# Optimization experiments

Measured on AMD Instinct MI355X. Metric: run time of the kernel, lower is better.

## Reference

```python
import jax, jax.numpy as jnp
import numpy as np

N, L, D, H = 2, 2048, 1024, 16
Dh = D // H          # 64
HIST = 2048          # history_len
SCALE = D ** 0.5     # note: module scales by sqrt(model_dim), not sqrt(head_dim)


def setup_inputs() -> dict:
    key = jax.random.key(0)
    ks = jax.random.split(key, 10)
    f = lambda k, s, sc=1.0: jax.random.normal(k, s, dtype=jnp.float32) * sc
    i = jnp.arange(L)
    causal = i[None, :] > i[:, None]            # mask future
    old = i[None, :] <= i[:, None] - HIST       # mask beyond history window
    mask = causal | old                          # True = masked, (L, L)
    return {
        "values": f(ks[0], (N, L, D)),
        "keys": f(ks[1], (N, L, D)),
        "query": f(ks[2], (N, L, D)),
        "origin_values": f(ks[3], (N, L, D)),
        "origin_keys": f(ks[4], (N, L, D)),
        "Wv": f(ks[5], (Dh, Dh), 0.1),
        "Wk": f(ks[6], (Dh, Dh), 0.1),
        "Wq": f(ks[7], (Dh, Dh), 0.1),
        "fc_w": f(ks[8], (D, D), 0.03),
        "fc_b": jnp.zeros((D,), dtype=jnp.float32),
        "mask": mask,
    }


def reference(values, keys, query, origin_values, origin_keys, Wv, Wk, Wq, fc_w, fc_b, mask):
    # forward(..., ref_sample=True): mfpca_attention path.
    # origin_keys/values are projected exactly as the prior ref_sample=False call stored them.
    split = lambda x: x.reshape(N, L, H, Dh)
    v = split(values) @ Wv.T        # (N, L, H, Dh)  torch Linear: x @ W^T, no bias
    k = split(keys) @ Wk.T
    q = split(query) @ Wq.T
    ov = split(origin_values) @ Wv.T
    ok = split(origin_keys) @ Wk.T

    energy = jnp.einsum('nqhd,nkhd->nhqk', q, ok)       # (N, H, L, L)
    samp_energy = jnp.einsum('nlhd,nlhd->nhl', q, k)    # (N, H, L)
    eye = jnp.eye(L, dtype=bool)
    # energy.diagonal().copy_(samp_energy)
    energy = jnp.where(eye, samp_energy[:, :, None, :], energy)
    energy = jnp.where(mask, jnp.float32(-1e20), energy)
    scores = jax.nn.softmax(energy / SCALE, axis=-1)
    diag_scores = jnp.diagonal(scores, axis1=2, axis2=3)    # (N, H, L)
    scores_nodiag = jnp.where(eye, 0.0, scores)
    # NOTE: original einsum output is indexed by l (not q) -- reproduced faithfully.
    origin_attention = jnp.einsum('nhql,nlhd->nlhd', scores_nodiag, ov)
    samp_attention = jnp.einsum('nhl,nlhd->nlhd', diag_scores, v)
    attention = (samp_attention + origin_attention).reshape(N, L, D)
    return attention @ fc_w.T + fc_b
```

## Files before the change

kernel.cpp:

```cpp
#include <hip/hip_runtime.h>

#define NB 2
#define LL 2048
#define DD 1024
#define HH 16
#define NHH (NB*HH)
#define LT (LL/64)
#define KT16 (LL/16)
#define CEXP 0.0450842200277801f

typedef __bf16 bf16x8 __attribute__((ext_vector_type(8)));
typedef unsigned short u16x8 __attribute__((ext_vector_type(8)));
typedef float f32x4 __attribute__((ext_vector_type(4)));

#define MFMA16 __builtin_amdgcn_mfma_f32_16x16x32_bf16
#define EXP2 __builtin_amdgcn_exp2f

__device__ __forceinline__ unsigned short f2bf(float f) {
    unsigned u = __float_as_uint(f);
    return (unsigned short)((u + 0x7fffu + ((u >> 16) & 1u)) >> 16);
}
__device__ __forceinline__ float bf2f(unsigned short u) {
    return __uint_as_float(((unsigned)u) << 16);
}
__device__ __forceinline__ bf16x8 ldfrag(const unsigned short* p) {
    return *reinterpret_cast<const bf16x8*>(p);
}
__device__ __forceinline__ bf16x8 cvt8v(float4 a, float4 b) {
    u16x8 u;
    u[0]=f2bf(a.x); u[1]=f2bf(a.y); u[2]=f2bf(a.z); u[3]=f2bf(a.w);
    u[4]=f2bf(b.x); u[5]=f2bf(b.y); u[6]=f2bf(b.z); u[7]=f2bf(b.w);
    return __builtin_bit_cast(bf16x8, u);
}
__device__ __forceinline__ ushort4 pack4(f32x4 d, float sc) {
    ushort4 o;
    o.x = f2bf(d[0]*sc); o.y = f2bf(d[1]*sc); o.z = f2bf(d[2]*sc); o.w = f2bf(d[3]*sc);
    return o;
}
__device__ __forceinline__ void gload16(const unsigned short* g, unsigned short* l) {
    __builtin_amdgcn_global_load_lds(
        (const __attribute__((address_space(1))) unsigned int*)g,
        (__attribute__((address_space(3))) unsigned int*)l, 16, 0, 0);
}

__global__ __launch_bounds__(256) void wcvt_kernel(
    const float* __restrict__ Wk, const float* __restrict__ Wq,
    const float* __restrict__ Wv, unsigned short* __restrict__ wfrag)
{
    const int s = blockIdx.x * 256 + threadIdx.x;
    const int m = s >> 9;
    const int rem = s & 511;
    const int f = rem >> 6;
    const int lane = rem & 63;
    const int n16 = lane & 15, quad = lane >> 4;
    const int mt = f >> 1, half = f & 1;
    const float* W = (m == 0) ? Wk : (m == 1) ? Wq : Wv;
    const float* p = W + (mt*16 + n16)*64 + quad*8 + half*32;
    float4 a = *reinterpret_cast<const float4*>(p);
    float4 b = *reinterpret_cast<const float4*>(p + 4);
    *reinterpret_cast<bf16x8*>(wfrag + (size_t)s * 8) = cvt8v(a, b);
}

__global__ __launch_bounds__(256) void proj_kernel(
    const float* __restrict__ values, const float* __restrict__ keys,
    const float* __restrict__ query,  const float* __restrict__ ovals,
    const float* __restrict__ okeys,  const unsigned short* __restrict__ wfrag,
    unsigned short* __restrict__ qb, unsigned short* __restrict__ okb,
    unsigned short* __restrict__ vb, unsigned short* __restrict__ ovb,
    float* __restrict__ ediag)
{
    const int t = threadIdx.x;
    const int w = t >> 6;
    const int lane = t & 63;
    const int n16 = lane & 15;
    const int quad = lane >> 4;
    const int h = blockIdx.y;
    const int row = blockIdx.x * 64 + w * 16 + n16;
    const int nn = row >> 11;
    const int ll = row & 2047;
    const size_t xoff  = (size_t)row * DD + h * 64 + quad * 8;
    const size_t qbase = (((size_t)(nn * HH + h)) * LL + ll) * 64;
    const size_t vbase = (size_t)row * DD + h * 64;

    if (blockIdx.z == 0) {
        const float4* kp = reinterpret_cast<const float4*>(keys  + xoff);
        const float4* qp = reinterpret_cast<const float4*>(query + xoff);
        const float4* op = reinterpret_cast<const float4*>(okeys + xoff);
        float4 k0 = kp[0], k1 = kp[1], k2 = kp[8], k3 = kp[9];
        float4 q0 = qp[0], q1 = qp[1], q2 = qp[8], q3 = qp[9];
        float4 o0 = op[0], o1 = op[1], o2 = op[8], o3 = op[9];
        bf16x8 wk[8], wq[8];
#pragma unroll
        for (int f = 0; f < 8; ++f) {
            wk[f] = ldfrag(wfrag + (size_t)(f * 64 + lane) * 8);
            wq[f] = ldfrag(wfrag + (size_t)((8 + f) * 64 + lane) * 8);
        }
        bf16x8 xk0 = cvt8v(k0, k1), xk1 = cvt8v(k2, k3);
        bf16x8 xq0 = cvt8v(q0, q1), xq1 = cvt8v(q2, q3);
        bf16x8 xo0 = cvt8v(o0, o1), xo1 = cvt8v(o2, o3);
        f32x4 ka[4], qa[4];
#pragma unroll
        for (int mt = 0; mt < 4; ++mt) {
            f32x4 d = {0.f,0.f,0.f,0.f};
            d = MFMA16(wk[mt*2], xk0, d, 0,0,0);
            ka[mt] = MFMA16(wk[mt*2+1], xk1, d, 0,0,0);
        }
#pragma unroll
        for (int mt = 0; mt < 4; ++mt) {
            f32x4 d = {0.f,0.f,0.f,0.f};
            d = MFMA16(wq[mt*2], xq0, d, 0,0,0);
            qa[mt] = MFMA16(wq[mt*2+1], xq1, d, 0,0,0);
            *reinterpret_cast<ushort4*>(qb + qbase + mt*16 + quad*4) = pack4(qa[mt], CEXP);
        }
#pragma unroll
        for (int mt = 0; mt < 4; ++mt) {
            f32x4 d = {0.f,0.f,0.f,0.f};
            d = MFMA16(wk[mt*2], xo0, d, 0,0,0);
            d = MFMA16(wk[mt*2+1], xo1, d, 0,0,0);
            *reinterpret_cast<ushort4*>(okb + qbase + mt*16 + quad*4) = pack4(d, 1.0f);
        }
        float p = 0.f;
#pragma unroll
        for (int mt = 0; mt < 4; ++mt)
            p += qa[mt][0]*ka[mt][0] + qa[mt][1]*ka[mt][1]
               + qa[mt][2]*ka[mt][2] + qa[mt][3]*ka[mt][3];
        p += __shfl_xor(p, 16);
        p += __shfl_xor(p, 32);
        if (lane < 16)
            ediag[((size_t)(nn * HH + h)) * LL + ll] = p;
    } else {
        const float4* vp = reinterpret_cast<const float4*>(values + xoff);
        const float4* op = reinterpret_cast<const float4*>(ovals  + xoff);
        float4 v0 = vp[0], v1 = vp[1], v2 = vp[8], v3 = vp[9];
        float4 o0 = op[0], o1 = op[1], o2 = op[8], o3 = op[9];
        bf16x8 wv[8];
#pragma unroll
        for (int f = 0; f < 8; ++f)
            wv[f] = ldfrag(wfrag + (size_t)((16 + f) * 64 + lane) * 8);
        bf16x8 xv0 = cvt8v(v0, v1), xv1 = cvt8v(v2, v3);
        bf16x8 xo0 = cvt8v(o0, o1), xo1 = cvt8v(o2, o3);
#pragma unroll
        for (int mt = 0; mt < 4; ++mt) {
            f32x4 d = {0.f,0.f,0.f,0.f};
            d = MFMA16(wv[mt*2], xv0, d, 0,0,0);
            d = MFMA16(wv[mt*2+1], xv1, d, 0,0,0);
            *reinterpret_cast<ushort4*>(vb + vbase + mt*16 + quad*4) = pack4(d, 1.0f);
        }
#pragma unroll
        for (int mt = 0; mt < 4; ++mt) {
            f32x4 d = {0.f,0.f,0.f,0.f};
            d = MFMA16(wv[mt*2], xo0, d, 0,0,0);
            d = MFMA16(wv[mt*2+1], xo1, d, 0,0,0);
            *reinterpret_cast<ushort4*>(ovb + vbase + mt*16 + quad*4) = pack4(d, 1.0f);
        }
    }
}

__global__ __launch_bounds__(256) void zrow_part(
    const unsigned short* __restrict__ qb, const unsigned short* __restrict__ okb,
    float* __restrict__ Zbuf)
{
    const int px = blockIdx.x;
    const int pair = px >> 1;
    const int s = px & 1;
    const int nh = blockIdx.y;
    const int t = threadIdx.x;
    const int w = t >> 6;
    const int lane = t & 63;
    const int n = lane & 15;
    const int quad = lane >> 4;
    const size_t base = (size_t)nh * (LL * 64);
    const size_t nhL = (size_t)nh * LL;
    const int r0 = 4 * s + w;

#pragma unroll
    for (int half = 0; half < 2; ++half) {
        const int qt = half ? (31 - pair) : pair;
        const int kend = 4 * qt + 4;

        bf16x8 bq[4][2];
#pragma unroll
        for (int ct = 0; ct < 4; ++ct) {
            const unsigned short* p = qb + base + (size_t)(qt*64 + ct*16 + n) * 64 + quad * 8;
            bq[ct][0] = ldfrag(p); bq[ct][1] = ldfrag(p + 32);
        }

        float zacc[4] = {0.f, 0.f, 0.f, 0.f};

        bf16x8 a0A = {}, a1A = {}, a0B = {}, a1B = {};
        if (r0 < kend) {
            const unsigned short* p = okb + base + (size_t)(r0*16 + n) * 64 + quad * 8;
            a0A = ldfrag(p); a1A = ldfrag(p + 32);
        }
        if (r0 + 8 < kend) {
            const unsigned short* p = okb + base + (size_t)((r0+8)*16 + n) * 64 + quad * 8;
            a0B = ldfrag(p); a1B = ldfrag(p + 32);
        }
        for (int kt = r0; kt < kend; kt += 8) {
            bf16x8 a0 = a0A, a1 = a1A;
            a0A = a0B; a1A = a1B;
            if (kt + 16 < kend) {
                const unsigned short* p = okb + base + (size_t)((kt+16)*16 + n) * 64 + quad * 8;
                a0B = ldfrag(p); a1B = ldfrag(p + 32);
            }
            const int dk = kt - 4*qt;
#pragma unroll
            for (int ct = 0; ct < 4; ++ct) {
                if (ct < dk) continue;
                f32x4 d = {0.f,0.f,0.f,0.f};
                d = MFMA16(a0, bq[ct][0], d, 0,0,0);
                d = MFMA16(a1, bq[ct][1], d, 0,0,0);
                if (ct == dk) {
#pragma unroll
                    for (int r = 0; r < 4; ++r)
                        if (quad*4 + r < n) zacc[ct] += EXP2(d[r]);
                } else {
#pragma unroll
                    for (int r = 0; r < 4; ++r) zacc[ct] += EXP2(d[r]);
                }
            }
        }

#pragma unroll
        for (int ct = 0; ct < 4; ++ct) {
            float z = zacc[ct];
            z += __shfl_down(z, 32);
            z += __shfl_down(z, 16);
            if (lane < 16)
                atomicAdd(&Zbuf[nhL + qt*64 + ct*16 + lane], z);
        }
    }
}

__global__ __launch_bounds__(256) void zfin_kernel(
    const float* __restrict__ Zbuf, const float* __restrict__ ediag,
    float* __restrict__ invZ, float* __restrict__ diag_s)
{
    const int i = blockIdx.x * 256 + threadIdx.x;
    const float de = EXP2(ediag[i] * CEXP);
    const float iz = 1.f / (Zbuf[i] + de);
    invZ[i]   = iz;
    diag_s[i] = de * iz;
}

__global__ __launch_bounds__(256) void colsum_part(
    const unsigned short* __restrict__ qb, const unsigned short* __restrict__ okb,
    const float* __restrict__ invZ, float* __restrict__ colsum)
{
    const int px = blockIdx.x;
    const int pair = px >> 1;
    const int s = px & 1;
    const int nh = blockIdx.y;
    const int t = threadIdx.x;
    const int w = t >> 6;
    const int lane = t & 63;
    const int n = lane & 15;
    const int quad = lane >> 4;
    const size_t base = (size_t)nh * (LL * 64);
    const size_t nhL = (size_t)nh * LL;
    const int r0 = 4 * s + w;

#pragma unroll
    for (int half = 0; half < 2; ++half) {
        const int lt = half ? (31 - pair) : pair;

        bf16x8 bl[4][2];
#pragma unroll
        for (int ct = 0; ct < 4; ++ct) {
            const unsigned short* p = okb + base + (size_t)(lt*64 + ct*16 + n) * 64 + quad * 8;
            bl[ct][0] = ldfrag(p); bl[ct][1] = ldfrag(p + 32);
        }

        float cacc[4] = {0.f, 0.f, 0.f, 0.f};

        const int kstart = 4*lt + r0;
        bf16x8 a0A = {}, a1A = {}, a0B = {}, a1B = {};
        float4 izA = {0.f,0.f,0.f,0.f}, izB = {0.f,0.f,0.f,0.f};
        if (kstart < KT16) {
            const unsigned short* p = qb + base + (size_t)(kstart*16 + n) * 64 + quad * 8;
            a0A = ldfrag(p); a1A = ldfrag(p + 32);
            izA = *reinterpret_cast<const float4*>(invZ + nhL + kstart*16 + quad*4);
        }
        if (kstart + 8 < KT16) {
            const unsigned short* p = qb + base + (size_t)((kstart+8)*16 + n) * 64 + quad * 8;
            a0B = ldfrag(p); a1B = ldfrag(p + 32);
            izB = *reinterpret_cast<const float4*>(invZ + nhL + (kstart+8)*16 + quad*4);
        }
        for (int kt = kstart; kt < KT16; kt += 8) {
            bf16x8 a0 = a0A, a1 = a1A; const float4 izv = izA;
            a0A = a0B; a1A = a1B; izA = izB;
            if (kt + 16 < KT16) {
                const unsigned short* p = qb + base + (size_t)((kt+16)*16 + n) * 64 + quad * 8;
                a0B = ldfrag(p); a1B = ldfrag(p + 32);
                izB = *reinterpret_cast<const float4*>(invZ + nhL + (kt+16)*16 + quad*4);
            }
            const int dk = kt - 4*lt;
#pragma unroll
            for (int ct = 0; ct < 4; ++ct) {
                if (ct > dk) continue;
                f32x4 d = {0.f,0.f,0.f,0.f};
                d = MFMA16(a0, bl[ct][0], d, 0,0,0);
                d = MFMA16(a1, bl[ct][1], d, 0,0,0);
                if (ct == dk) {
                    if (quad*4 + 0 > n) cacc[ct] += EXP2(d[0]) * izv.x;
                    if (quad*4 + 1 > n) cacc[ct] += EXP2(d[1]) * izv.y;
                    if (quad*4 + 2 > n) cacc[ct] += EXP2(d[2]) * izv.z;
                    if (quad*4 + 3 > n) cacc[ct] += EXP2(d[3]) * izv.w;
                } else {
                    cacc[ct] += EXP2(d[0]) * izv.x;
                    cacc[ct] += EXP2(d[1]) * izv.y;
                    cacc[ct] += EXP2(d[2]) * izv.z;
                    cacc[ct] += EXP2(d[3]) * izv.w;
                }
            }
        }

#pragma unroll
        for (int ct = 0; ct < 4; ++ct) {
            float c = cacc[ct];
            c += __shfl_down(c, 32);
            c += __shfl_down(c, 16);
            if (lane < 16)
                atomicAdd(&colsum[nhL + lt*64 + ct*16 + lane], c);
        }
    }
}

__global__ __launch_bounds__(256) void fcw_kernel(
    const float* __restrict__ fc_w, unsigned short* __restrict__ fcwb)
{
    const int idx = blockIdx.x * 1024 + threadIdx.x * 4;
    float4 wv = *reinterpret_cast<const float4*>(fc_w + idx);
    ushort4 o;
    o.x = f2bf(wv.x); o.y = f2bf(wv.y); o.z = f2bf(wv.z); o.w = f2bf(wv.w);
    *reinterpret_cast<ushort4*>(fcwb + idx) = o;
}

__global__ __launch_bounds__(256) void att_kernel(
    const unsigned short* __restrict__ vb, const unsigned short* __restrict__ ovb,
    const float* __restrict__ diag_s, const float* __restrict__ colsum,
    unsigned short* __restrict__ attb)
{
    const int row = blockIdx.x;
    const int nn = row >> 11, l = row & 2047;
    const int t = threadIdx.x;
    const int d0 = t * 4;
    const int h = t >> 4;
    const size_t nhl = ((size_t)(nn * HH + h)) * LL + l;
    const float ds = diag_s[nhl];
    const float cs = colsum[nhl];
    const ushort4 v  = *reinterpret_cast<const ushort4*>(vb  + (size_t)row * DD + d0);
    const ushort4 ov = *reinterpret_cast<const ushort4*>(ovb + (size_t)row * DD + d0);
    ushort4 o;
    o.x = f2bf(ds * bf2f(v.x) + cs * bf2f(ov.x));
    o.y = f2bf(ds * bf2f(v.y) + cs * bf2f(ov.y));
    o.z = f2bf(ds * bf2f(v.z) + cs * bf2f(ov.z));
    o.w = f2bf(ds * bf2f(v.w) + cs * bf2f(ov.w));
    *reinterpret_cast<ushort4*>(attb + (size_t)row * DD + d0) = o;
}

__global__ __launch_bounds__(512) void out_kernel(
    const unsigned short* __restrict__ attb, const unsigned short* __restrict__ fcwb,
    const float* __restrict__ fc_b, float* __restrict__ out)
{
    __shared__ unsigned short lds[2][2][128 * 32];

    const int bid = blockIdx.x;
    const int swz = (bid & 7) * 32 + (bid >> 3);
    const int ct = swz & 7;
    const int rt = swz >> 3;
    const int row0 = rt * 128, col0 = ct * 128;

    const int t = threadIdx.x;
    const int w = t >> 6, lane = t & 63;
    const int n = lane & 15, quad = lane >> 4;
    const int wr = w >> 2, wc = w & 3;

    const unsigned short* ga = attb + (size_t)(row0 + (t >> 2)) * DD + (t & 3) * 8;
    const unsigned short* gb = fcwb + (size_t)(col0 + (t >> 2)) * DD + (t & 3) * 8;
    unsigned short* la0 = &lds[0][0][t * 8];
    unsigned short* lb0 = &lds[0][1][t * 8];
    unsigned short* la1 = &lds[1][0][t * 8];
    unsigned short* lb1 = &lds[1][1][t * 8];

    f32x4 acc[4][2];
#pragma unroll
    for (int mt = 0; mt < 4; ++mt)
#pragma unroll
        for (int nt = 0; nt < 2; ++nt) acc[mt][nt] = (f32x4){0.f, 0.f, 0.f, 0.f};

    gload16(ga, la0);
    gload16(gb, lb0);
    __syncthreads();

    int cur = 0;
    for (int kt = 0; kt < DD / 32; ++kt) {
        if (kt + 1 < DD / 32) {
            const int kc = (kt + 1) * 32;
            gload16(ga + kc, cur ? la0 : la1);
            gload16(gb + kc, cur ? lb0 : lb1);
        }
        const unsigned short* A = &lds[cur][0][0];
        const unsigned short* B = &lds[cur][1][0];
        bf16x8 af[4], bf_[2];
#pragma unroll
        for (int mt = 0; mt < 4; ++mt)
            af[mt] = ldfrag(A + (wr * 64 + mt * 16 + n) * 32 + quad * 8);
#pragma unroll
        for (int nt = 0; nt < 2; ++nt)
            bf_[nt] = ldfrag(B + (wc * 32 + nt * 16 + n) * 32 + quad * 8);
#pragma unroll
        for (int mt = 0; mt < 4; ++mt)
#pragma unroll
            for (int nt = 0; nt < 2; ++nt)
                acc[mt][nt] = MFMA16(af[mt], bf_[nt], acc[mt][nt], 0, 0, 0);
        __syncthreads();
        cur ^= 1;
    }

#pragma unroll
    for (int nt = 0; nt < 2; ++nt) {
        const int col = col0 + wc * 32 + nt * 16 + n;
        const float bias = fc_b[col];
#pragma unroll
        for (int mt = 0; mt < 4; ++mt)
#pragma unroll
            for (int r = 0; r < 4; ++r)
                out[(size_t)(row0 + wr * 64 + mt * 16 + quad * 4 + r) * DD + col]
                    = acc[mt][nt][r] + bias;
    }
}

extern "C" void kernel_launch(void* const* d_in, const int* in_sizes, int n_in,
                              void* d_out, int out_size, void* d_ws, size_t ws_size,
                              hipStream_t stream) {
    const float* values = (const float*)d_in[0];
    const float* keys   = (const float*)d_in[1];
    const float* query  = (const float*)d_in[2];
    const float* ovals  = (const float*)d_in[3];
    const float* okeys  = (const float*)d_in[4];
    const float* Wv     = (const float*)d_in[5];
    const float* Wk     = (const float*)d_in[6];
    const float* Wq     = (const float*)d_in[7];
    const float* fc_w   = (const float*)d_in[8];
    const float* fc_b   = (const float*)d_in[9];
    float* out = (float*)d_out;

    float* ws      = (float*)d_ws;
    float* ediag   = ws;
    float* Zbuf    = ediag + 65536;
    float* colsum  = Zbuf + 65536;
    float* invZ    = colsum + 65536;
    float* diag_s  = invZ + 65536;
    unsigned short* qb   = (unsigned short*)(diag_s + 65536);
    unsigned short* okb  = qb   + 4194304;
    unsigned short* vb   = okb  + 4194304;
    unsigned short* ovb  = vb   + 4194304;
    unsigned short* attb = ovb  + 4194304;
    unsigned short* fcwb = attb + 4194304;
    unsigned short* wfrag = fcwb + 1048576;

    hipMemsetAsync(Zbuf, 0, 2 * 65536 * sizeof(float), stream);

    wcvt_kernel<<<dim3(6), 256, 0, stream>>>(Wk, Wq, Wv, wfrag);
    fcw_kernel<<<dim3(1024), 256, 0, stream>>>(fc_w, fcwb);
    proj_kernel<<<dim3(64, 16, 2), 256, 0, stream>>>(
        values, keys, query, ovals, okeys, wfrag, qb, okb, vb, ovb, ediag);
    zrow_part<<<dim3(32, NHH), 256, 0, stream>>>(qb, okb, Zbuf);
    zfin_kernel<<<dim3(256), 256, 0, stream>>>(Zbuf, ediag, invZ, diag_s);
    colsum_part<<<dim3(32, NHH), 256, 0, stream>>>(qb, okb, invZ, colsum);
    att_kernel<<<dim3(NB * LL), 256, 0, stream>>>(vb, ovb, diag_s, colsum, attb);
    out_kernel<<<dim3(256), 512, 0, stream>>>(attb, fcwb, fc_b, out);
}
```

Before: 239.1 us.

## Fuse attention combine into output GEMM, merge prep kernels, deepen prefetch

Removes the separate att_kernel by computing ds*v + cs*ov on the fly while staging the A tile of the final fc GEMM, so the intermediate attb buffer is never written or read back. Weight conversion, fc_w conversion and the Z/colsum zeroing are merged into one prep kernel, which drops two launches and a memset. The zrow and colsum loops now prefetch three k-tiles ahead instead of two. The GEMM A path changes from async global-to-LDS loads to register loads plus conversion, which raises register pressure and can stall the main loop.

```diff
diff --git a/kernel.cpp b/kernel.cpp
--- a/kernel.cpp
+++ b/kernel.cpp
@@ -43,22 +43,37 @@
         (__attribute__((address_space(3))) unsigned int*)l, 16, 0, 0);
 }
 
-__global__ __launch_bounds__(256) void wcvt_kernel(
+__global__ __launch_bounds__(256) void prep_kernel(
     const float* __restrict__ Wk, const float* __restrict__ Wq,
-    const float* __restrict__ Wv, unsigned short* __restrict__ wfrag)
-{
-    const int s = blockIdx.x * 256 + threadIdx.x;
-    const int m = s >> 9;
-    const int rem = s & 511;
-    const int f = rem >> 6;
-    const int lane = rem & 63;
-    const int n16 = lane & 15, quad = lane >> 4;
-    const int mt = f >> 1, half = f & 1;
-    const float* W = (m == 0) ? Wk : (m == 1) ? Wq : Wv;
-    const float* p = W + (mt*16 + n16)*64 + quad*8 + half*32;
-    float4 a = *reinterpret_cast<const float4*>(p);
-    float4 b = *reinterpret_cast<const float4*>(p + 4);
-    *reinterpret_cast<bf16x8*>(wfrag + (size_t)s * 8) = cvt8v(a, b);
+    const float* __restrict__ Wv, unsigned short* __restrict__ wfrag,
+    const float* __restrict__ fc_w, unsigned short* __restrict__ fcwb,
+    float* __restrict__ zreg)
+{
+    const int bid = blockIdx.x;
+    const int t = threadIdx.x;
+    if (bid < 6) {
+        const int s = bid * 256 + t;
+        const int m = s >> 9;
+        const int rem = s & 511;
+        const int f = rem >> 6;
+        const int lane = rem & 63;
+        const int n16 = lane & 15, quad = lane >> 4;
+        const int mt = f >> 1, half = f & 1;
+        const float* W = (m == 0) ? Wk : (m == 1) ? Wq : Wv;
+        const float* p = W + (mt*16 + n16)*64 + quad*8 + half*32;
+        float4 a = *reinterpret_cast<const float4*>(p);
+        float4 b = *reinterpret_cast<const float4*>(p + 4);
+        *reinterpret_cast<bf16x8*>(wfrag + (size_t)s * 8) = cvt8v(a, b);
+    } else if (bid < 6 + 1024) {
+        const int idx = (bid - 6) * 1024 + t * 4;
+        float4 wv = *reinterpret_cast<const float4*>(fc_w + idx);
+        ushort4 o;
+        o.x = f2bf(wv.x); o.y = f2bf(wv.y); o.z = f2bf(wv.z); o.w = f2bf(wv.w);
+        *reinterpret_cast<ushort4*>(fcwb + idx) = o;
+    } else {
+        const int i = (bid - 1030) * 1024 + t * 4;
+        *reinterpret_cast<float4*>(zreg + i) = (float4){0.f, 0.f, 0.f, 0.f};
+    }
 }
 
 __global__ __launch_bounds__(256) void proj_kernel(
@@ -187,7 +202,7 @@
 
         float zacc[4] = {0.f, 0.f, 0.f, 0.f};
 
-        bf16x8 a0A = {}, a1A = {}, a0B = {}, a1B = {};
+        bf16x8 a0A = {}, a1A = {}, a0B = {}, a1B = {}, a0C = {}, a1C = {};
         if (r0 < kend) {
             const unsigned short* p = okb + base + (size_t)(r0*16 + n) * 64 + quad * 8;
             a0A = ldfrag(p); a1A = ldfrag(p + 32);
@@ -196,12 +211,16 @@
             const unsigned short* p = okb + base + (size_t)((r0+8)*16 + n) * 64 + quad * 8;
             a0B = ldfrag(p); a1B = ldfrag(p + 32);
         }
+        if (r0 + 16 < kend) {
+            const unsigned short* p = okb + base + (size_t)((r0+16)*16 + n) * 64 + quad * 8;
+            a0C = ldfrag(p); a1C = ldfrag(p + 32);
+        }
         for (int kt = r0; kt < kend; kt += 8) {
             bf16x8 a0 = a0A, a1 = a1A;
-            a0A = a0B; a1A = a1B;
-            if (kt + 16 < kend) {
-                const unsigned short* p = okb + base + (size_t)((kt+16)*16 + n) * 64 + quad * 8;
-                a0B = ldfrag(p); a1B = ldfrag(p + 32);
+            a0A = a0B; a1A = a1B; a0B = a0C; a1B = a1C;
+            if (kt + 24 < kend) {
+                const unsigned short* p = okb + base + (size_t)((kt+24)*16 + n) * 64 + quad * 8;
+                a0C = ldfrag(p); a1C = ldfrag(p + 32);
             }
             const int dk = kt - 4*qt;
 #pragma unroll
@@ -274,8 +293,8 @@
         float cacc[4] = {0.f, 0.f, 0.f, 0.f};
 
         const int kstart = 4*lt + r0;
-        bf16x8 a0A = {}, a1A = {}, a0B = {}, a1B = {};
-        float4 izA = {0.f,0.f,0.f,0.f}, izB = {0.f,0.f,0.f,0.f};
+        bf16x8 a0A = {}, a1A = {}, a0B = {}, a1B = {}, a0C = {}, a1C = {};
+        float4 izA = {0,0,0,0}, izB = {0,0,0,0}, izC = {0,0,0,0};
         if (kstart < KT16) {
             const unsigned short* p = qb + base + (size_t)(kstart*16 + n) * 64 + quad * 8;
             a0A = ldfrag(p); a1A = ldfrag(p + 32);
@@ -286,13 +305,19 @@
             a0B = ldfrag(p); a1B = ldfrag(p + 32);
             izB = *reinterpret_cast<const float4*>(invZ + nhL + (kstart+8)*16 + quad*4);
         }
+        if (kstart + 16 < KT16) {
+            const unsigned short* p = qb + base + (size_t)((kstart+16)*16 + n) * 64 + quad * 8;
+            a0C = ldfrag(p); a1C = ldfrag(p + 32);
+            izC = *reinterpret_cast<const float4*>(invZ + nhL + (kstart+16)*16 + quad*4);
+        }
         for (int kt = kstart; kt < KT16; kt += 8) {
             bf16x8 a0 = a0A, a1 = a1A; const float4 izv = izA;
             a0A = a0B; a1A = a1B; izA = izB;
-            if (kt + 16 < KT16) {
-                const unsigned short* p = qb + base + (size_t)((kt+16)*16 + n) * 64 + quad * 8;
-                a0B = ldfrag(p); a1B = ldfrag(p + 32);
-                izB = *reinterpret_cast<const float4*>(invZ + nhL + (kt+16)*16 + quad*4);
+            a0B = a0C; a1B = a1C; izB = izC;
+            if (kt + 24 < KT16) {
+                const unsigned short* p = qb + base + (size_t)((kt+24)*16 + n) * 64 + quad * 8;
+                a0C = ldfrag(p); a1C = ldfrag(p + 32);
+                izC = *reinterpret_cast<const float4*>(invZ + nhL + (kt+24)*16 + quad*4);
             }
             const int dk = kt - 4*lt;
 #pragma unroll
@@ -326,42 +351,43 @@
     }
 }
 
-__global__ __launch_bounds__(256) void fcw_kernel(
-    const float* __restrict__ fc_w, unsigned short* __restrict__ fcwb)
-{
-    const int idx = blockIdx.x * 1024 + threadIdx.x * 4;
-    float4 wv = *reinterpret_cast<const float4*>(fc_w + idx);
-    ushort4 o;
-    o.x = f2bf(wv.x); o.y = f2bf(wv.y); o.z = f2bf(wv.z); o.w = f2bf(wv.w);
-    *reinterpret_cast<ushort4*>(fcwb + idx) = o;
-}
-
-__global__ __launch_bounds__(256) void att_kernel(
+#define LOADA(vS, ovS, dsS, csS, k) do {                                   \
+    vS  = ldfrag(pv  + (k)*32);                                            \
+    ovS = ldfrag(pov + (k)*32);                                            \
+    dsS = diag_s[scbase + ((k)>>1)*LL];                                    \
+    csS = colsum[scbase + ((k)>>1)*LL];                                    \
+} while (0)
+
+#define CVTWRITE(vS, ovS, dsS, csS, dst) do {                              \
+    u16x8 vu_ = __builtin_bit_cast(u16x8, vS);                             \
+    u16x8 ou_ = __builtin_bit_cast(u16x8, ovS);                            \
+    u16x8 o_;                                                              \
+    _Pragma("unroll")                                                      \
+    for (int i_ = 0; i_ < 8; ++i_)                                         \
+        o_[i_] = f2bf(dsS * bf2f(vu_[i_]) + csS * bf2f(ou_[i_]));          \
+    *reinterpret_cast<u16x8*>(dst) = o_;                                   \
+} while (0)
+
+#define COMPUTE(Abuf, Bbuf) do {                                           \
+    bf16x8 af_[4], bf_[2];                                                 \
+    _Pragma("unroll")                                                      \
+    for (int mt = 0; mt < 4; ++mt)                                         \
+        af_[mt] = ldfrag((Abuf) + (wr*64 + mt*16 + n)*32 + quad*8);        \
+    _Pragma("unroll")                                                      \
+    for (int nt = 0; nt < 2; ++nt)                                         \
+        bf_[nt] = ldfrag((Bbuf) + (wc*32 + nt*16 + n)*32 + quad*8);        \
+    _Pragma("unroll")                                                      \
+    for (int mt = 0; mt < 4; ++mt)                                         \
+        _Pragma("unroll")                                                  \
+        for (int nt = 0; nt < 2; ++nt)                                     \
+            acc[mt][nt] = MFMA16(af_[mt], bf_[nt], acc[mt][nt], 0,0,0);    \
+} while (0)
+
+__global__ __launch_bounds__(512) void out_kernel(
     const unsigned short* __restrict__ vb, const unsigned short* __restrict__ ovb,
     const float* __restrict__ diag_s, const float* __restrict__ colsum,
-    unsigned short* __restrict__ attb)
-{
-    const int row = blockIdx.x;
-    const int nn = row >> 11, l = row & 2047;
-    const int t = threadIdx.x;
-    const int d0 = t * 4;
-    const int h = t >> 4;
-    const size_t nhl = ((size_t)(nn * HH + h)) * LL + l;
-    const float ds = diag_s[nhl];
-    const float cs = colsum[nhl];
-    const ushort4 v  = *reinterpret_cast<const ushort4*>(vb  + (size_t)row * DD + d0);
-    const ushort4 ov = *reinterpret_cast<const ushort4*>(ovb + (size_t)row * DD + d0);
-    ushort4 o;
-    o.x = f2bf(ds * bf2f(v.x) + cs * bf2f(ov.x));
-    o.y = f2bf(ds * bf2f(v.y) + cs * bf2f(ov.y));
-    o.z = f2bf(ds * bf2f(v.z) + cs * bf2f(ov.z));
-    o.w = f2bf(ds * bf2f(v.w) + cs * bf2f(ov.w));
-    *reinterpret_cast<ushort4*>(attb + (size_t)row * DD + d0) = o;
-}
-
-__global__ __launch_bounds__(512) void out_kernel(
-    const unsigned short* __restrict__ attb, const unsigned short* __restrict__ fcwb,
-    const float* __restrict__ fc_b, float* __restrict__ out)
+    const unsigned short* __restrict__ fcwb, const float* __restrict__ fc_b,
+    float* __restrict__ out)
 {
     __shared__ unsigned short lds[2][2][128 * 32];
 
@@ -376,12 +402,19 @@
     const int n = lane & 15, quad = lane >> 4;
     const int wr = w >> 2, wc = w & 3;
 
-    const unsigned short* ga = attb + (size_t)(row0 + (t >> 2)) * DD + (t & 3) * 8;
+    const int arow = row0 + (t >> 2);
+    const unsigned short* pv  = vb  + (size_t)arow * DD + (t & 3) * 8;
+    const unsigned short* pov = ovb + (size_t)arow * DD + (t & 3) * 8;
+    const int scbase = (arow >> 11) * (HH * LL) + (arow & 2047);
     const unsigned short* gb = fcwb + (size_t)(col0 + (t >> 2)) * DD + (t & 3) * 8;
     unsigned short* la0 = &lds[0][0][t * 8];
     unsigned short* lb0 = &lds[0][1][t * 8];
     unsigned short* la1 = &lds[1][0][t * 8];
     unsigned short* lb1 = &lds[1][1][t * 8];
+    const unsigned short* A0 = &lds[0][0][0];
+    const unsigned short* B0 = &lds[0][1][0];
+    const unsigned short* A1 = &lds[1][0][0];
+    const unsigned short* B1 = &lds[1][1][0];
 
     f32x4 acc[4][2];
 #pragma unroll
@@ -389,33 +422,26 @@
 #pragma unroll
         for (int nt = 0; nt < 2; ++nt) acc[mt][nt] = (f32x4){0.f, 0.f, 0.f, 0.f};
 
-    gload16(ga, la0);
+    bf16x8 vP, ovP, vQ, ovQ; float dsP, csP, dsQ, csQ;
+    LOADA(vP, ovP, dsP, csP, 0);
+    LOADA(vQ, ovQ, dsQ, csQ, 1);
     gload16(gb, lb0);
+    CVTWRITE(vP, ovP, dsP, csP, la0);
     __syncthreads();
 
-    int cur = 0;
-    for (int kt = 0; kt < DD / 32; ++kt) {
-        if (kt + 1 < DD / 32) {
-            const int kc = (kt + 1) * 32;
-            gload16(ga + kc, cur ? la0 : la1);
-            gload16(gb + kc, cur ? lb0 : lb1);
-        }
-        const unsigned short* A = &lds[cur][0][0];
-        const unsigned short* B = &lds[cur][1][0];
-        bf16x8 af[4], bf_[2];
-#pragma unroll
-        for (int mt = 0; mt < 4; ++mt)
-            af[mt] = ldfrag(A + (wr * 64 + mt * 16 + n) * 32 + quad * 8);
-#pragma unroll
-        for (int nt = 0; nt < 2; ++nt)
-            bf_[nt] = ldfrag(B + (wc * 32 + nt * 16 + n) * 32 + quad * 8);
-#pragma unroll
-        for (int mt = 0; mt < 4; ++mt)
-#pragma unroll
-            for (int nt = 0; nt < 2; ++nt)
-                acc[mt][nt] = MFMA16(af[mt], bf_[nt], acc[mt][nt], 0, 0, 0);
+    for (int kt = 0; kt < 32; kt += 2) {
+        gload16(gb + (kt + 1) * 32, lb1);
+        if (kt + 2 < 32) LOADA(vP, ovP, dsP, csP, kt + 2);
+        COMPUTE(A0, B0);
+        CVTWRITE(vQ, ovQ, dsQ, csQ, la1);
         __syncthreads();
-        cur ^= 1;
+        if (kt + 2 < 32) {
+            gload16(gb + (kt + 2) * 32, lb0);
+            if (kt + 3 < 32) LOADA(vQ, ovQ, dsQ, csQ, kt + 3);
+        }
+        COMPUTE(A1, B1);
+        if (kt + 2 < 32) CVTWRITE(vP, ovP, dsP, csP, la0);
+        __syncthreads();
     }
 
 #pragma unroll
@@ -456,19 +482,14 @@
     unsigned short* okb  = qb   + 4194304;
     unsigned short* vb   = okb  + 4194304;
     unsigned short* ovb  = vb   + 4194304;
-    unsigned short* attb = ovb  + 4194304;
-    unsigned short* fcwb = attb + 4194304;
+    unsigned short* fcwb = ovb  + 4194304;
     unsigned short* wfrag = fcwb + 1048576;
 
-    hipMemsetAsync(Zbuf, 0, 2 * 65536 * sizeof(float), stream);
-
-    wcvt_kernel<<<dim3(6), 256, 0, stream>>>(Wk, Wq, Wv, wfrag);
-    fcw_kernel<<<dim3(1024), 256, 0, stream>>>(fc_w, fcwb);
+    prep_kernel<<<dim3(1158), 256, 0, stream>>>(Wk, Wq, Wv, wfrag, fc_w, fcwb, Zbuf);
     proj_kernel<<<dim3(64, 16, 2), 256, 0, stream>>>(
         values, keys, query, ovals, okeys, wfrag, qb, okb, vb, ovb, ediag);
     zrow_part<<<dim3(32, NHH), 256, 0, stream>>>(qb, okb, Zbuf);
     zfin_kernel<<<dim3(256), 256, 0, stream>>>(Zbuf, ediag, invZ, diag_s);
     colsum_part<<<dim3(32, NHH), 256, 0, stream>>>(qb, okb, invZ, colsum);
-    att_kernel<<<dim3(NB * LL), 256, 0, stream>>>(vb, ovb, diag_s, colsum, attb);
-    out_kernel<<<dim3(256), 512, 0, stream>>>(attb, fcwb, fc_b, out);
-}
+    out_kernel<<<dim3(256), 512, 0, stream>>>(vb, ovb, diag_s, colsum, fcwb, fc_b, out);
+}
```

New measurement: 237.8 us. Within noise of the previous version (-0.5%).
